# Performance work log

Measured on AMD Instinct MI355X. Metric: run time of the kernel, lower is better.

The kernel has to match this reference:

```python
import jax, jax.numpy as jnp
import numpy as np

NUM_TOKENS = 8192
TOKEN_DIM = 256
N = 65536
TOPK = 5
DECAY = 0.1      # cur_decay (set_decay_updates never called -> stays at init decay)
EPS = 1e-5
TEMP = 1.0


def setup_inputs() -> dict:
    key = jax.random.key(0)
    k1, k2 = jax.random.split(key)
    return {
        "inputs_flatten": jax.random.normal(k1, (N, TOKEN_DIM), dtype=jnp.float32),
        "embed": jax.random.normal(k2, (NUM_TOKENS, TOKEN_DIM), dtype=jnp.float32),
        "cluster_size": jnp.zeros((NUM_TOKENS,), dtype=jnp.float32),
        "cluster_sum": jnp.zeros((NUM_TOKENS,), dtype=jnp.float32),
        "embed_avg": jnp.zeros((NUM_TOKENS, TOKEN_DIM), dtype=jnp.float32),
    }


def reference(inputs_flatten, embed, cluster_size, cluster_sum, embed_avg):
    x = inputs_flatten                              # [N, D]
    # squared euclidean distances to codebook: [N, K]
    distances = (jnp.sum(x * x, axis=1, keepdims=True)
                 + jnp.sum(embed * embed, axis=1)
                 - 2.0 * (x @ embed.T))
    # top-k nearest codes (smallest distance)
    neg_topk, topk_idx = jax.lax.top_k(-distances, TOPK)   # [N, k]
    topk_dist = -neg_topk
    weights = jax.nn.softmax(-topk_dist / TEMP, axis=1)    # [N, k]
    # scatter soft weights into dense one-hot-ish encodings [N, K]
    rows = jnp.arange(x.shape[0])[:, None]
    encodings = jnp.zeros_like(distances).at[rows, topk_idx].set(weights)
    encoding_indices = jnp.argmax(encodings, axis=1)[:, None]   # [N, 1]

    # training-mode EMA codebook update (module default is training=True)
    encoding_sum = jnp.sum(encodings, axis=0)                   # [K]
    new_cluster_sum = cluster_sum + encoding_sum
    new_cluster_size = cluster_size * DECAY + encoding_sum * (1.0 - DECAY)
    embed_sum = encodings.T @ x                                 # [K, D]
    new_embed_avg = embed_avg * DECAY + embed_sum * (1.0 - DECAY)
    smoothed = (new_cluster_size + EPS) / (jnp.sum(new_cluster_size) + NUM_TOKENS * EPS)
    cs = smoothed * jnp.sum(new_cluster_size)
    new_embed = new_embed_avg / cs[:, None]                     # embed.data.copy_(...)

    quantize = encodings @ new_embed                            # [N, D]
    quantize = jax.lax.stop_gradient(quantize - x) + x          # straight-through
    return quantize, encoding_indices
```

## Files before the change

kernel.cpp:

```cpp
#include <hip/hip_runtime.h>
#include <hip/hip_bf16.h>
#include <math.h>
#include <limits.h>

#define NROWS 65536
#define DIM   256
#define NCODE 8192
#define NTOPK 5

typedef __attribute__((ext_vector_type(4))) float     f32x4;
typedef __attribute__((ext_vector_type(4))) int       i32x4;
typedef __attribute__((ext_vector_type(2))) unsigned  u32x2;

#define WS_ESWZ   0u
#define WS_CINIT  2097152u
#define WS_CAND   2129920u
#define WS_IDX5   4227072u
#define WS_W5     5537792u
#define WS_ENCSUM 6848512u
#define WS_CNT    6881280u
#define WS_OFFS   6914048u
#define WS_CURS   6946816u
#define WS_SFAC   6979584u
#define WS_ENTR   6979840u
#define WS_NEWEMB 9601280u

#define ENT_PER_BLK 64
#define NENT (NROWS * NTOPK)

__device__ __forceinline__ void gl_lds16(const void* g, void* l) {
  __builtin_amdgcn_global_load_lds(
      (const __attribute__((address_space(1))) unsigned int*)g,
      (__attribute__((address_space(3))) unsigned int*)l, 16, 0, 0);
}

__device__ __forceinline__ unsigned f2key(float f) {
  unsigned u = __float_as_uint(f);
  return (u & 0x80000000u) ? ~u : (u | 0x80000000u);
}
__device__ __forceinline__ float key2f(unsigned k) {
  unsigned u = (k & 0x80000000u) ? (k ^ 0x80000000u) : ~k;
  return __uint_as_float(u);
}

__global__ __launch_bounds__(256) void k_prep(const float* __restrict__ embed,
                                              signed char* __restrict__ eswz,
                                              int* __restrict__ cinit) {
  const int code = blockIdx.x;
  const int d = threadIdx.x;
  float v = embed[code * DIM + d];
  float qf = fminf(127.f, fmaxf(-127.f, rintf(16.f * v)));
  int q = (int)qf;
  __shared__ unsigned char rb[256];
  __shared__ int red[4];
  rb[d] = (unsigned char)(q & 255);
  int e2 = q * q;
  #pragma unroll
  for (int off = 32; off; off >>= 1) e2 += __shfl_down(e2, off);
  const int lane = d & 63, w = d >> 6;
  if (lane == 0) red[w] = e2;
  __syncthreads();
  if (d == 0) cinit[code] = -((red[0] + red[1] + red[2] + red[3]) >> 1);
  if (d < 64) {
    unsigned u = (unsigned)rb[4 * d] | ((unsigned)rb[4 * d + 1] << 8) |
                 ((unsigned)rb[4 * d + 2] << 16) | ((unsigned)rb[4 * d + 3] << 24);
    const int cs = (d >> 2) ^ (code & 15);
    ((unsigned*)(eswz + code * 256))[(cs << 2) | (d & 3)] = u;
  }
}


struct PList { int a, b, c, d; };

__device__ __forceinline__ void ladder(PList& P, int t) {
  int c0 = min(P.a, t); P.a = max(P.a, t);
  int c1 = min(P.b, c0); P.b = max(P.b, c0);
  int c2 = min(P.c, c1); P.c = max(P.c, c1);
  P.d = max(P.d, c2);
}

__device__ __forceinline__ void psel(PList& P, i32x4 acc, int cb) {
  int p0 = (acc[0] << 13) + cb;
  int p1 = (acc[1] << 13) + cb + 1;
  int p2 = (acc[2] << 13) + cb + 2;
  int p3 = (acc[3] << 13) + cb + 3;
  int h1 = max(p0, p1), l1 = min(p0, p1);
  int h2 = max(p2, p3), l2 = min(p2, p3);
  int t1 = max(h1, h2);
  int t2 = max(min(h1, h2), max(l1, l2));
  ladder(P, t1);
  if (__any(t2 > P.d)) ladder(P, t2);
}

__device__ __forceinline__ int pk4(f32x4 v) {
  int r = 0;
  #pragma unroll
  for (int j = 0; j < 4; ++j) {
    float q = fminf(127.f, fmaxf(-127.f, rintf(16.f * v[j])));
    r |= ((int)q & 255) << (8 * j);
  }
  return r;
}

__global__ __launch_bounds__(256, 2) void k_gemm(const float* __restrict__ x,
                                                 const signed char* __restrict__ eswz,
                                                 const int* __restrict__ cinit,
                                                 unsigned short* __restrict__ cand) {
  __shared__ signed char ebuf[3][8192];
  __shared__ int ci_s[NCODE];
  const int tid = threadIdx.x;
  const int lane = tid & 63, wave = tid >> 6;
  const int q = lane >> 4, ln = lane & 15;
  const int wrow0 = blockIdx.x * 128 + wave * 32;

  #pragma unroll
  for (int r = 0; r < 8; ++r)
    gl_lds16(cinit + r * 1024 + tid * 4, &ci_s[r * 1024 + tid * 4]);
  gl_lds16(eswz + tid * 16, &ebuf[0][tid * 16]);
  gl_lds16(eswz + 4096 + tid * 16, &ebuf[0][4096 + tid * 16]);

  i32x4 xf[2][4];
  #pragma unroll
  for (int t = 0; t < 2; ++t) {
    const float* xr = x + (unsigned)(wrow0 + t * 16 + ln) * DIM;
    #pragma unroll
    for (int s = 0; s < 4; ++s) {
      i32x4 dw;
      #pragma unroll
      for (int d = 0; d < 4; ++d)
        dw[d] = pk4(*(const f32x4*)(xr + s * 64 + q * 16 + d * 4));
      xf[t][s] = dw;
    }
  }

  PList P0 = {INT_MIN, INT_MIN, INT_MIN, INT_MIN};
  PList P1 = P0;

  int slot = 0;
  #pragma unroll 1
  for (int it = 0; it < 256; ++it) {
    const int nslot = (slot + 1 == 3) ? 0 : slot + 1;
    const int tl = (it < 255) ? it + 1 : 255;
    const signed char* src = eswz + (unsigned)tl * 8192;
    gl_lds16(src + tid * 16, &ebuf[nslot][tid * 16]);
    gl_lds16(src + 4096 + tid * 16, &ebuf[nslot][4096 + tid * 16]);

    asm volatile("s_waitcnt vmcnt(2)\n\ts_barrier" ::: "memory");

    #pragma unroll
    for (int c = 0; c < 2; ++c) {
      const int cbase = it * 32 + c * 16 + q * 4;
      i32x4 en = *(const i32x4*)&ci_s[cbase];
      i32x4 acc0 = en, acc1 = en;
      const signed char* eb = &ebuf[slot][c * 4096];
      #pragma unroll
      for (int s = 0; s < 4; ++s) {
        const int chunk = (4 * s + q) ^ ln;
        i32x4 ea = *(const i32x4*)&eb[ln * 256 + chunk * 16];
        acc0 = __builtin_amdgcn_mfma_i32_16x16x64_i8(ea, xf[0][s], acc0, 0, 0, 0);
        acc1 = __builtin_amdgcn_mfma_i32_16x16x64_i8(ea, xf[1][s], acc1, 0, 0, 0);
      }
      psel(P0, acc0, cbase);
      psel(P1, acc1, cbase);
    }
    slot = nslot;
  }

  {
    const int row0 = wrow0 + ln;
    u32x2 pk;
    pk[0] = ((unsigned)P0.a & 8191u) | (((unsigned)P0.b & 8191u) << 16);
    pk[1] = ((unsigned)P0.c & 8191u) | (((unsigned)P0.d & 8191u) << 16);
    *(u32x2*)&cand[row0 * 16 + q * 4] = pk;
    const int row1 = wrow0 + 16 + ln;
    pk[0] = ((unsigned)P1.a & 8191u) | (((unsigned)P1.b & 8191u) << 16);
    pk[1] = ((unsigned)P1.c & 8191u) | (((unsigned)P1.d & 8191u) << 16);
    *(u32x2*)&cand[row1 * 16 + q * 4] = pk;
  }
}

__global__ __launch_bounds__(256) void k_refine(const float* __restrict__ x,
                                                const float* __restrict__ embed,
                                                const unsigned short* __restrict__ cand,
                                                float* __restrict__ out_idx,
                                                int* __restrict__ idx5,
                                                float* __restrict__ w5,
                                                float* __restrict__ enc_sum,
                                                unsigned* __restrict__ cnt) {
  __shared__ float sh[4][16][66];
  const int wave = threadIdx.x >> 6, l = threadIdx.x & 63;
  const int row = blockIdx.x * 4 + wave;
  const float* xr = x + (unsigned)row * DIM;
  const float t0 = -2.f * xr[l], t1 = -2.f * xr[l + 64];
  const float t2 = -2.f * xr[l + 128], t3 = -2.f * xr[l + 192];

  int cd[16];
  const unsigned* cp = (const unsigned*)(cand + row * 16);
  #pragma unroll
  for (int i = 0; i < 8; ++i) {
    unsigned v = cp[i];
    cd[2 * i] = (int)(v & 0xFFFFu);
    cd[2 * i + 1] = (int)(v >> 16);
  }

  #pragma unroll
  for (int ci = 0; ci < 16; ++ci) {
    const float* er = embed + (unsigned)cd[ci] * DIM;
    const float e0 = er[l], e1 = er[l + 64], e2 = er[l + 128], e3 = er[l + 192];
    float p = e0 * (e0 + t0);
    p = fmaf(e1, e1 + t1, p);
    p = fmaf(e2, e2 + t2, p);
    p = fmaf(e3, e3 + t3, p);
    sh[wave][ci][l] = p;
  }
  asm volatile("s_waitcnt lgkmcnt(0)" ::: "memory");

  const int c = l >> 2, sub = l & 3;
  const float* sp = &sh[wave][c][sub * 16];
  double s64 = 0.0;
  #pragma unroll
  for (int i = 0; i < 4; ++i) {
    f32x4 v = *(const f32x4*)(sp + i * 4);
    s64 += (double)v[0] + (double)v[1] + (double)v[2] + (double)v[3];
  }
  s64 += __shfl_xor(s64, 1);
  s64 += __shfl_xor(s64, 2);

  double sc = __shfl(s64, (l & 15) * 4);
  unsigned key = f2key((float)sc);
  const int myc = cd[l & 15];

  bool used = false;
  int codes[5]; float svals[5];
  #pragma unroll
  for (int j = 0; j < 5; ++j) {
    unsigned k = used ? 0xFFFFFFFFu : key;
    unsigned mm = k;
    #pragma unroll
    for (int off = 1; off < 16; off <<= 1) mm = min(mm, (unsigned)__shfl_xor((int)mm, off));
    int cc = (k == mm) ? myc : 0x7FFFFFFF;
    #pragma unroll
    for (int off = 1; off < 16; off <<= 1) cc = min(cc, __shfl_xor(cc, off));
    used = used || (myc == cc);
    codes[j] = cc;
    svals[j] = key2f(mm);
  }

  float ex[5], sum = 0.f;
  #pragma unroll
  for (int j = 0; j < 5; ++j) { ex[j] = expf(-(svals[j] - svals[0])); sum += ex[j]; }
  const float inv = 1.f / sum;

  if (l == 0) {
    out_idx[row] = (float)codes[0];
    #pragma unroll
    for (int j = 0; j < 5; ++j) {
      float w = ex[j] * inv;
      idx5[row * 5 + j] = codes[j];
      w5[row * 5 + j] = w;
      atomicAdd(&enc_sum[codes[j]], w);
      atomicAdd(&cnt[codes[j]], 1u);
    }
  }
}

__global__ __launch_bounds__(256) void k_scan(const unsigned* __restrict__ cnt,
                                              unsigned* __restrict__ offs,
                                              unsigned* __restrict__ cursor,
                                              const float* __restrict__ enc_sum,
                                              const float* __restrict__ cluster_size,
                                              float* __restrict__ sfac) {
  __shared__ unsigned part[256];
  __shared__ double sred[256];
  const int t = threadIdx.x;
  unsigned s = 0;
  for (int i = 0; i < 32; ++i) s += cnt[t * 32 + i];
  part[t] = s;
  double ds = 0.0;
  for (int i = t; i < NCODE; i += 256)
    ds += 0.1 * (double)cluster_size[i] + 0.9 * (double)enc_sum[i];
  sred[t] = ds;
  __syncthreads();
  if (t == 0) {
    unsigned run = 0;
    for (int i = 0; i < 256; ++i) { unsigned tmp = part[i]; part[i] = run; run += tmp; }
    double S = 0.0;
    for (int i = 0; i < 256; ++i) S += sred[i];
    sfac[0] = (float)(S / (S + (double)NCODE * 1e-5));
  }
  __syncthreads();
  unsigned off = part[t];
  for (int i = 0; i < 32; ++i) {
    unsigned c = cnt[t * 32 + i];
    offs[t * 32 + i] = off;
    cursor[t * 32 + i] = off;
    off += c;
  }
}

__global__ __launch_bounds__(256) void k_fill(const int* __restrict__ idx5,
                                              const float* __restrict__ w5,
                                              unsigned* __restrict__ cursor,
                                              uint2* __restrict__ entries) {
  const int i = blockIdx.x * 256 + threadIdx.x;
  if (i >= NENT) return;
  const unsigned c = (unsigned)idx5[i];
  const float w = w5[i];
  const unsigned row = (unsigned)i / 5u;
  const unsigned slot = atomicAdd(&cursor[c], 1u);
  entries[slot] = make_uint2((c << 16) | row, __float_as_uint(w));
}

__global__ __launch_bounds__(256) void k_accum2(const float* __restrict__ x,
                                                const uint2* __restrict__ entries,
                                                float* __restrict__ embsum) {
  __shared__ uint2 ent[ENT_PER_BLK];
  const int t = threadIdx.x;
  const unsigned base = blockIdx.x * ENT_PER_BLK;
  if (t < ENT_PER_BLK * 2)
    ((unsigned*)ent)[t] = ((const unsigned*)(entries + base))[t];
  __syncthreads();

  float acc = 0.f;
  unsigned cur = ent[0].x >> 16;
  #pragma unroll 8
  for (int i = 0; i < ENT_PER_BLK; ++i) {
    const uint2 e = ent[i];
    const unsigned code = e.x >> 16;
    const unsigned row = e.x & 0xFFFFu;
    const float w = __uint_as_float(e.y);
    if (code != cur) {
      atomicAdd(&embsum[cur * DIM + t], acc);
      acc = 0.f; cur = code;
    }
    acc = fmaf(w, x[row * DIM + t], acc);
  }
  atomicAdd(&embsum[cur * DIM + t], acc);
}

__global__ __launch_bounds__(256) void k_norm(const float* __restrict__ embed_avg,
                                              const float* __restrict__ cluster_size,
                                              const float* __restrict__ enc_sum,
                                              const float* __restrict__ sfac,
                                              float* __restrict__ embsum ) {
  const int k = blockIdx.x, d = threadIdx.x;
  const float ncs = 0.1f * cluster_size[k] + 0.9f * enc_sum[k];
  const float cs = (ncs + 1e-5f) * sfac[0];
  const unsigned o = (unsigned)k * DIM + d;
  embsum[o] = (0.1f * embed_avg[o] + 0.9f * embsum[o]) / cs;
}

__global__ __launch_bounds__(256) void k_quant(const int* __restrict__ idx5,
                                               const float* __restrict__ w5,
                                               const float* __restrict__ newemb,
                                               float* __restrict__ out) {
  const int d = threadIdx.x;
  const int rb = blockIdx.x * 16;
  #pragma unroll 2
  for (int r = 0; r < 16; ++r) {
    const int row = rb + r;
    float acc = 0.f;
    #pragma unroll
    for (int j = 0; j < 5; ++j)
      acc = fmaf(w5[row * 5 + j], newemb[(unsigned)idx5[row * 5 + j] * DIM + d], acc);
    out[(unsigned)row * DIM + d] = acc;
  }
}

extern "C" void kernel_launch(void* const* d_in, const int* in_sizes, int n_in,
                              void* d_out, int out_size, void* d_ws, size_t ws_size,
                              hipStream_t stream) {
  const float* x            = (const float*)d_in[0];
  const float* embed        = (const float*)d_in[1];
  const float* cluster_size = (const float*)d_in[2];
  const float* embed_avg    = (const float*)d_in[4];

  char* w = (char*)d_ws;
  signed char*    eswz   = (signed char*)(w + WS_ESWZ);
  int*            cinit  = (int*)(w + WS_CINIT);
  unsigned short* cand   = (unsigned short*)(w + WS_CAND);
  int*            idx5   = (int*)(w + WS_IDX5);
  float*          w5     = (float*)(w + WS_W5);
  float*          encsum = (float*)(w + WS_ENCSUM);
  unsigned*       cnt    = (unsigned*)(w + WS_CNT);
  unsigned*       offs   = (unsigned*)(w + WS_OFFS);
  unsigned*       curs   = (unsigned*)(w + WS_CURS);
  float*          sfac   = (float*)(w + WS_SFAC);
  uint2*          entr   = (uint2*)(w + WS_ENTR);
  float*          embsum = (float*)(w + WS_NEWEMB);

  float* out_q   = (float*)d_out;
  float* out_idx = out_q + (size_t)NROWS * DIM;

  hipMemsetAsync(w + WS_ENCSUM, 0, 65536, stream);
  hipMemsetAsync(w + WS_NEWEMB, 0, (size_t)NCODE * DIM * 4, stream);

  k_prep<<<NCODE, 256, 0, stream>>>(embed, eswz, cinit);
  k_gemm<<<512, 256, 0, stream>>>(x, eswz, cinit, cand);
  k_refine<<<NROWS / 4, 256, 0, stream>>>(x, embed, cand, out_idx, idx5, w5, encsum, cnt);
  k_scan<<<1, 256, 0, stream>>>(cnt, offs, curs, encsum, cluster_size, sfac);
  k_fill<<<(NENT + 255) / 256, 256, 0, stream>>>(idx5, w5, curs, entr);
  k_accum2<<<NENT / ENT_PER_BLK, 256, 0, stream>>>(x, entr, embsum);
  k_norm<<<NCODE, 256, 0, stream>>>(embed_avg, cluster_size, encsum, sfac, embsum);
  k_quant<<<NROWS / 16, 256, 0, stream>>>(idx5, w5, embsum, out_q);
}
```

Measured before the change: 485.5 us.

## Restructure int8 GEMM for one row tile per wave and higher occupancy

The int8 screening GEMM now gives each wave 16 rows instead of 32, splitting each 32-code tile across two accumulators that are merged at the end. It drops the 32KB LDS copy of code norms, prefetching per-tile norms from global into registers instead. This raises the occupancy target from 2 to 4 blocks per CU. The refine kernel switches to float4 vectorized loads of x and embed rows. The trade-off is twice as many blocks re-streaming the whole codebook from L2, and less MFMA reuse of each codebook fragment.

```diff
diff --git a/kernel.cpp b/kernel.cpp
--- a/kernel.cpp
+++ b/kernel.cpp
@@ -79,11 +79,11 @@
   P.d = max(P.d, c2);
 }
 
-__device__ __forceinline__ void psel(PList& P, i32x4 acc, int cb) {
-  int p0 = (acc[0] << 13) + cb;
-  int p1 = (acc[1] << 13) + cb + 1;
-  int p2 = (acc[2] << 13) + cb + 2;
-  int p3 = (acc[3] << 13) + cb + 3;
+__device__ __forceinline__ void psel(PList& P, i32x4 acc, i32x4 en, int cb) {
+  int p0 = ((acc[0] + en[0]) << 13) + cb;
+  int p1 = ((acc[1] + en[1]) << 13) + cb + 1;
+  int p2 = ((acc[2] + en[2]) << 13) + cb + 2;
+  int p3 = ((acc[3] + en[3]) << 13) + cb + 3;
   int h1 = max(p0, p1), l1 = min(p0, p1);
   int h2 = max(p2, p3), l2 = min(p2, p3);
   int t1 = max(h1, h2);
@@ -102,34 +102,32 @@
   return r;
 }
 
-__global__ __launch_bounds__(256, 2) void k_gemm(const float* __restrict__ x,
+__global__ __launch_bounds__(256, 4) void k_gemm(const float* __restrict__ x,
                                                  const signed char* __restrict__ eswz,
                                                  const int* __restrict__ cinit,
                                                  unsigned short* __restrict__ cand) {
   __shared__ signed char ebuf[3][8192];
-  __shared__ int ci_s[NCODE];
   const int tid = threadIdx.x;
   const int lane = tid & 63, wave = tid >> 6;
   const int q = lane >> 4, ln = lane & 15;
-  const int wrow0 = blockIdx.x * 128 + wave * 32;
-
-  #pragma unroll
-  for (int r = 0; r < 8; ++r)
-    gl_lds16(cinit + r * 1024 + tid * 4, &ci_s[r * 1024 + tid * 4]);
+  const int row = blockIdx.x * 64 + wave * 16 + ln;
+
   gl_lds16(eswz + tid * 16, &ebuf[0][tid * 16]);
   gl_lds16(eswz + 4096 + tid * 16, &ebuf[0][4096 + tid * 16]);
 
-  i32x4 xf[2][4];
-  #pragma unroll
-  for (int t = 0; t < 2; ++t) {
-    const float* xr = x + (unsigned)(wrow0 + t * 16 + ln) * DIM;
+  i32x4 enc0 = *(const i32x4*)(cinit + q * 4);
+  i32x4 enc1 = *(const i32x4*)(cinit + 16 + q * 4);
+
+  i32x4 xf[4];
+  {
+    const float* xr = x + (unsigned)row * DIM;
     #pragma unroll
     for (int s = 0; s < 4; ++s) {
       i32x4 dw;
       #pragma unroll
       for (int d = 0; d < 4; ++d)
         dw[d] = pk4(*(const f32x4*)(xr + s * 64 + q * 16 + d * 4));
-      xf[t][s] = dw;
+      xf[s] = dw;
     }
   }
 
@@ -144,39 +142,34 @@
     const signed char* src = eswz + (unsigned)tl * 8192;
     gl_lds16(src + tid * 16, &ebuf[nslot][tid * 16]);
     gl_lds16(src + 4096 + tid * 16, &ebuf[nslot][4096 + tid * 16]);
-
-    asm volatile("s_waitcnt vmcnt(2)\n\ts_barrier" ::: "memory");
-
-    #pragma unroll
-    for (int c = 0; c < 2; ++c) {
-      const int cbase = it * 32 + c * 16 + q * 4;
-      i32x4 en = *(const i32x4*)&ci_s[cbase];
-      i32x4 acc0 = en, acc1 = en;
-      const signed char* eb = &ebuf[slot][c * 4096];
-      #pragma unroll
-      for (int s = 0; s < 4; ++s) {
-        const int chunk = (4 * s + q) ^ ln;
-        i32x4 ea = *(const i32x4*)&eb[ln * 256 + chunk * 16];
-        acc0 = __builtin_amdgcn_mfma_i32_16x16x64_i8(ea, xf[0][s], acc0, 0, 0, 0);
-        acc1 = __builtin_amdgcn_mfma_i32_16x16x64_i8(ea, xf[1][s], acc1, 0, 0, 0);
-      }
-      psel(P0, acc0, cbase);
-      psel(P1, acc1, cbase);
+    i32x4 enn0 = *(const i32x4*)(cinit + tl * 32 + q * 4);
+    i32x4 enn1 = *(const i32x4*)(cinit + tl * 32 + 16 + q * 4);
+
+    asm volatile("s_waitcnt vmcnt(4)\n\ts_barrier" ::: "memory");
+
+    const signed char* eb = ebuf[slot];
+    i32x4 acc0 = {0, 0, 0, 0}, acc1 = {0, 0, 0, 0};
+    #pragma unroll
+    for (int s = 0; s < 4; ++s) {
+      const int chunk = (4 * s + q) ^ ln;
+      i32x4 ea0 = *(const i32x4*)&eb[ln * 256 + chunk * 16];
+      i32x4 ea1 = *(const i32x4*)&eb[4096 + ln * 256 + chunk * 16];
+      acc0 = __builtin_amdgcn_mfma_i32_16x16x64_i8(ea0, xf[s], acc0, 0, 0, 0);
+      acc1 = __builtin_amdgcn_mfma_i32_16x16x64_i8(ea1, xf[s], acc1, 0, 0, 0);
     }
+    psel(P0, acc0, enc0, it * 32 + q * 4);
+    psel(P1, acc1, enc1, it * 32 + 16 + q * 4);
+
+    enc0 = enn0; enc1 = enn1;
     slot = nslot;
   }
 
-  {
-    const int row0 = wrow0 + ln;
-    u32x2 pk;
-    pk[0] = ((unsigned)P0.a & 8191u) | (((unsigned)P0.b & 8191u) << 16);
-    pk[1] = ((unsigned)P0.c & 8191u) | (((unsigned)P0.d & 8191u) << 16);
-    *(u32x2*)&cand[row0 * 16 + q * 4] = pk;
-    const int row1 = wrow0 + 16 + ln;
-    pk[0] = ((unsigned)P1.a & 8191u) | (((unsigned)P1.b & 8191u) << 16);
-    pk[1] = ((unsigned)P1.c & 8191u) | (((unsigned)P1.d & 8191u) << 16);
-    *(u32x2*)&cand[row1 * 16 + q * 4] = pk;
-  }
+  ladder(P0, P1.a); ladder(P0, P1.b); ladder(P0, P1.c); ladder(P0, P1.d);
+
+  u32x2 pk;
+  pk[0] = ((unsigned)P0.a & 8191u) | (((unsigned)P0.b & 8191u) << 16);
+  pk[1] = ((unsigned)P0.c & 8191u) | (((unsigned)P0.d & 8191u) << 16);
+  *(u32x2*)&cand[row * 16 + q * 4] = pk;
 }
 
 __global__ __launch_bounds__(256) void k_refine(const float* __restrict__ x,
@@ -191,8 +184,9 @@
   const int wave = threadIdx.x >> 6, l = threadIdx.x & 63;
   const int row = blockIdx.x * 4 + wave;
   const float* xr = x + (unsigned)row * DIM;
-  const float t0 = -2.f * xr[l], t1 = -2.f * xr[l + 64];
-  const float t2 = -2.f * xr[l + 128], t3 = -2.f * xr[l + 192];
+  const f32x4 xv = *(const f32x4*)(xr + 4 * l);
+  const float t0 = -2.f * xv[0], t1 = -2.f * xv[1];
+  const float t2 = -2.f * xv[2], t3 = -2.f * xv[3];
 
   int cd[16];
   const unsigned* cp = (const unsigned*)(cand + row * 16);
@@ -205,12 +199,11 @@
 
   #pragma unroll
   for (int ci = 0; ci < 16; ++ci) {
-    const float* er = embed + (unsigned)cd[ci] * DIM;
-    const float e0 = er[l], e1 = er[l + 64], e2 = er[l + 128], e3 = er[l + 192];
-    float p = e0 * (e0 + t0);
-    p = fmaf(e1, e1 + t1, p);
-    p = fmaf(e2, e2 + t2, p);
-    p = fmaf(e3, e3 + t3, p);
+    const f32x4 e = *(const f32x4*)(embed + (unsigned)cd[ci] * DIM + 4 * l);
+    float p = e[0] * (e[0] + t0);
+    p = fmaf(e[1], e[1] + t1, p);
+    p = fmaf(e[2], e[2] + t2, p);
+    p = fmaf(e[3], e[3] + t3, p);
     sh[wave][ci][l] = p;
   }
   asm volatile("s_waitcnt lgkmcnt(0)" ::: "memory");
@@ -396,7 +389,7 @@
   hipMemsetAsync(w + WS_NEWEMB, 0, (size_t)NCODE * DIM * 4, stream);
 
   k_prep<<<NCODE, 256, 0, stream>>>(embed, eswz, cinit);
-  k_gemm<<<512, 256, 0, stream>>>(x, eswz, cinit, cand);
+  k_gemm<<<NROWS / 64, 256, 0, stream>>>(x, eswz, cinit, cand);
   k_refine<<<NROWS / 4, 256, 0, stream>>>(x, embed, cand, out_idx, idx5, w5, encsum, cnt);
   k_scan<<<1, 256, 0, stream>>>(cnt, offs, curs, encsum, cluster_size, sfac);
   k_fill<<<(NENT + 255) / 256, 256, 0, stream>>>(idx5, w5, curs, entr);
```

New measurement: 489.3 us. About the same (+0.8%).
